# Kernel optimization log

Measured on AMD Instinct MI355X. Metric: run time of the kernel, lower is better.

Reference implementation:

```python
import jax, jax.numpy as jnp
import numpy as np

T_HORIZON = 200

def setup_inputs() -> dict:
    key = jax.random.key(0)
    ks = jax.random.split(key, 6)
    B, x_dim, kdim, u_dim = 131072, 128, 256, 64
    return {
        "x0": jax.random.normal(ks[0], (B, x_dim), jnp.float32),
        "W_phi": jax.random.normal(ks[1], (kdim, x_dim), jnp.float32) / np.float32(np.sqrt(x_dim)),
        "b_phi": jnp.zeros((kdim,), jnp.float32),
        "x_goal": jax.random.normal(ks[2], (x_dim,), jnp.float32),
        # scaled so the 200-step Riccati recursion stays numerically sane in fp32
        "phi_affine": jax.random.normal(ks[3], (kdim, kdim), jnp.float32) * np.float32(0.9 / np.sqrt(kdim)),
        "u_affine": jax.random.normal(ks[4], (kdim, u_dim), jnp.float32),
        "q_diag_log": jnp.zeros((kdim,), jnp.float32),
        "r_diag_log": jnp.zeros((u_dim,), jnp.float32),
    }

def reference(x0, W_phi, b_phi, x_goal, phi_affine, u_affine, q_diag_log, r_diag_log):
    A = phi_affine            # (k,k)
    Bm = u_affine             # (k,u)
    At, Bt = A.T, Bm.T
    Q = jnp.diag(jnp.exp(q_diag_log))   # (k,k)
    R = jnp.diag(jnp.exp(r_diag_log))   # (u,u)
    goal_g = W_phi @ x_goal + b_phi     # phi(x_goal), (k,)

    def riccati_step(carry, _):
        V, v = carry                                   # (k,k), (k,)
        M = Bt @ (V @ Bm) + R                          # (u,u)
        S = jnp.linalg.solve(M, Bt)                    # V_uu^-1 B^T, (u,k)
        K = S @ (V @ A)                                # (u,k)
        kv = S @ v                                     # (u,)
        A_BK = A - Bm @ K                              # (k,k)
        V_new = At @ (V @ A_BK) + Q
        v_new = A_BK.T @ v + Q @ goal_g
        return (V_new, v_new), (K, kv)

    (_, _), (Ks, kvs) = jax.lax.scan(riccati_step, (Q, Q @ goal_g), None, length=T_HORIZON)
    K0, k0 = Ks[-1], kvs[-1]   # last scan iter corresponds to i=0 of the reversed torch loop

    g0 = x0 @ W_phi.T + b_phi  # phi(x0), (B,k)
    u = -(g0 @ K0.T) + k0      # (B,u)
    return u
```

## Files before the change

kernel.cpp:

```cpp
#include <hip/hip_runtime.h>
#include <math.h>

#define KD 256
#define UD 64
#define XD 128

#define OFF_V     0
#define OFF_WA    65536
#define OFF_H     131072
#define OFF_G     196608
#define OFF_K0    212992
#define OFF_MI    229376
#define OFF_MP    233472
#define OFF_v     266240
#define OFF_ATV   266496
#define OFF_Z     266752
#define OFF_QG    266816
#define OFF_QD    267072
#define OFF_RD    267328
#define OFF_KV    267392
#define OFF_CV    267456
#define OFF_NKT   267520
#define DBASE     139264
#define DBUF      65536

__device__ __forceinline__ void inv4(float* D) {
#pragma unroll
  for (int p = 0; p < 4; ++p) {
    float ip = 1.0f / D[p * 4 + p];
#pragma unroll
    for (int i2 = 0; i2 < 4; ++i2)
      if (i2 != p) {
        float f = D[i2 * 4 + p] * ip;
#pragma unroll
        for (int j = 0; j < 4; ++j)
          if (j != p) D[i2 * 4 + j] -= f * D[p * 4 + j];
        D[i2 * 4 + p] = -f;
      }
#pragma unroll
    for (int j = 0; j < 4; ++j)
      if (j != p) D[p * 4 + j] *= ip;
    D[p * 4 + p] = ip;
  }
}

__device__ __forceinline__ void inv4d(double* D) {
#pragma unroll
  for (int p = 0; p < 4; ++p) {
    double ip = 1.0 / D[p * 4 + p];
#pragma unroll
    for (int i2 = 0; i2 < 4; ++i2)
      if (i2 != p) {
        double f = D[i2 * 4 + p] * ip;
#pragma unroll
        for (int j = 0; j < 4; ++j)
          if (j != p) D[i2 * 4 + j] -= f * D[p * 4 + j];
        D[i2 * 4 + p] = -f;
      }
#pragma unroll
    for (int j = 0; j < 4; ++j)
      if (j != p) D[p * 4 + j] *= ip;
    D[p * 4 + p] = ip;
  }
}

#define R16(OP) OP(0) OP(1) OP(2) OP(3) OP(4) OP(5) OP(6) OP(7) OP(8) OP(9) OP(10) OP(11) OP(12) OP(13) OP(14) OP(15)

__global__ __launch_bounds__(256) void k_init(
    const float* __restrict__ W, const float* __restrict__ bphi,
    const float* __restrict__ xg, const float* __restrict__ qlog,
    const float* __restrict__ rlog, float* __restrict__ ws)
{
  const int w = blockIdx.x, t = threadIdx.x;
  if (w < 4 && t < 64) {
    int i = w * 64 + t;
    float acc = 0.f;
    for (int p = 0; p < XD; ++p) acc = fmaf(W[i * XD + p], xg[p], acc);
    float g = acc + bphi[i];
    float qd = expf(qlog[i]);
    ws[OFF_QD + i] = qd; ws[OFF_QG + i] = qd * g; ws[OFF_v + i] = qd * g;
  }
  if (w == 4 && t < UD) ws[OFF_RD + t] = expf(rlog[t]);
}

__global__ __launch_bounds__(256) void k_cvt(
    const float* __restrict__ A, const float* __restrict__ B, float* __restrict__ ws)
{
  double* base = (double*)ws + DBASE;
  double* E1 = base + 0 * DBUF;
  double* H1 = base + 2 * DBUF;
  double* MB = base + 14 * DBUF;
  double* B64 = MB;
  double* Bs64 = MB + 16384;
  double* eA = MB + 32768;
  double* hA = MB + 33024;
  int id = blockIdx.x * 256 + threadIdx.x;
  E1[id] = (double)A[id];
  int i = id >> 8, j = id & 255;
  H1[id] = (i == j) ? (double)ws[OFF_QD + i] : 0.0;
  if (id < 16384) {
    int m = id & 63;
    B64[id] = (double)B[id];
    Bs64[id] = (double)B[id] / (double)ws[OFF_RD + m];
  }
  if (id < 256) {
    eA[id] = 0.0;
    hA[id] = -(double)ws[OFF_QG + id];
  }
}

struct GJ { const double* A; const double* B; const double* C; double* O;
            int sA0, sA1, sB0, sB1, K, addI; };
struct VJ { const double* M1; const double* x; const double* a; double* o;
            int s0, s1; double sgn; };

__global__ __launch_bounds__(256) void k_gemm64(GJ g0, GJ g1, GJ g2, int ng,
                                                VJ v0, VJ v1, VJ v2)
{
  __shared__ double As[32 * 33];
  __shared__ double Bs[32 * 33];
  __shared__ double xs[256];
  const int wg = blockIdx.x, t = threadIdx.x;
  if (wg < ng * 64) {
    GJ j = (wg < 64) ? g0 : (wg < 128) ? g1 : g2;
    const int w2 = wg & 63;
    const int tm0 = (w2 >> 3) * 32, tn0 = (w2 & 7) * 32;
    const int rq = t >> 5, c = t & 31;
    double a0 = 0, a1 = 0, a2 = 0, a3 = 0;
    for (int k0 = 0; k0 < j.K; k0 += 32) {
#pragma unroll
      for (int q = 0; q < 4; ++q) {
        int lin = q * 256 + t; int r = lin >> 5, kk = lin & 31;
        As[r * 33 + kk] = j.A[(long)(tm0 + r) * j.sA0 + (long)(k0 + kk) * j.sA1];
        Bs[r * 33 + kk] = j.B[(long)(k0 + r) * j.sB0 + (long)(tn0 + kk) * j.sB1];
      }
      __syncthreads();
#pragma unroll 8
      for (int kk = 0; kk < 32; ++kk) {
        double b = Bs[kk * 33 + c];
        a0 = fma(As[(rq * 4 + 0) * 33 + kk], b, a0);
        a1 = fma(As[(rq * 4 + 1) * 33 + kk], b, a1);
        a2 = fma(As[(rq * 4 + 2) * 33 + kk], b, a2);
        a3 = fma(As[(rq * 4 + 3) * 33 + kk], b, a3);
      }
      __syncthreads();
    }
    const int n = tn0 + c;
    double av[4] = {a0, a1, a2, a3};
#pragma unroll
    for (int i2 = 0; i2 < 4; ++i2) {
      int m = tm0 + rq * 4 + i2;
      double v = av[i2];
      if (j.C) v += j.C[m * 256 + n];
      if (j.addI && m == n) v += 1.0;
      j.O[m * 256 + n] = v;
    }
  } else {
    const int vi = wg - ng * 64;
    VJ j = (vi == 0) ? v0 : (vi == 1) ? v1 : v2;
    xs[t] = j.x[t];
    __syncthreads();
    double acc = 0;
#pragma unroll 8
    for (int k2 = 0; k2 < 256; ++k2)
      acc = fma(j.M1[(long)t * j.s0 + (long)k2 * j.s1], xs[k2], acc);
    double o = j.sgn * acc;
    if (j.a) o += j.a[t];
    j.o[t] = o;
  }
}

__global__ __launch_bounds__(256) void k_pinv(const double* __restrict__ Yc,
                                              double* __restrict__ Yn, int pk)
{
  const int w = blockIdx.x, t = threadIdx.x;
  const int bi = w >> 3, bj = w & 7;
  const int p0 = pk * 64, pb = pk * 2;
  const int r0 = bi * 32, c0 = bj * 32;

  __shared__ double sDI[64 * 65];
  __shared__ double sC [32 * 66];
  __shared__ double sR [64 * 34];
  __shared__ double sL [32 * 66];
  __shared__ double sU [64 * 34];
  __shared__ double sPR[4 * 68];
  __shared__ double sF [64 * 5];

  for (int q = 0; q < 8; ++q) { int lin = q * 256 + t; int r = lin >> 6, m = lin & 63; sC[r * 66 + m] = Yc[(r0 + r) * 256 + p0 + m]; }
  for (int q = 0; q < 8; ++q) { int lin = q * 256 + t; int m = lin >> 5, c = lin & 31; sR[m * 34 + c] = Yc[(p0 + m) * 256 + c0 + c]; }

  const int i = t & 63, cg = t >> 6;
  double rr[16];
#pragma unroll
  for (int q = 0; q < 16; ++q) rr[q] = Yc[(p0 + i) * 256 + p0 + cg * 16 + q];
  for (int k = 0; k < 16; ++k) {
    const int prw = i - 4 * k;
    const bool inblk = (unsigned)prw < 4u;
    if (inblk) {
#pragma unroll
      for (int q = 0; q < 16; ++q) sPR[prw * 68 + cg * 16 + q] = rr[q];
    }
    if (cg == (k >> 2)) {
      const int b = (k & 3) * 4;
      sF[i * 5 + 0] = rr[b + 0]; sF[i * 5 + 1] = rr[b + 1];
      sF[i * 5 + 2] = rr[b + 2]; sF[i * 5 + 3] = rr[b + 3];
    }
    __syncthreads();
    double D[16];
#pragma unroll
    for (int q = 0; q < 4; ++q) {
      D[q * 4 + 0] = sPR[q * 68 + 4 * k + 0];
      D[q * 4 + 1] = sPR[q * 68 + 4 * k + 1];
      D[q * 4 + 2] = sPR[q * 68 + 4 * k + 2];
      D[q * 4 + 3] = sPR[q * 68 + 4 * k + 3];
    }
    inv4d(D);
    double f0 = sF[i * 5 + 0], f1 = sF[i * 5 + 1], f2 = sF[i * 5 + 2], f3 = sF[i * 5 + 3];
    double g0, g1, g2, g3;
    if (inblk) {
      g0 = prw == 0 ? D[0] : prw == 1 ? D[4] : prw == 2 ? D[8]  : D[12];
      g1 = prw == 0 ? D[1] : prw == 1 ? D[5] : prw == 2 ? D[9]  : D[13];
      g2 = prw == 0 ? D[2] : prw == 1 ? D[6] : prw == 2 ? D[10] : D[14];
      g3 = prw == 0 ? D[3] : prw == 1 ? D[7] : prw == 2 ? D[11] : D[15];
    } else {
      g0 = f0 * D[0] + f1 * D[4] + f2 * D[8]  + f3 * D[12];
      g1 = f0 * D[1] + f1 * D[5] + f2 * D[9]  + f3 * D[13];
      g2 = f0 * D[2] + f1 * D[6] + f2 * D[10] + f3 * D[14];
      g3 = f0 * D[3] + f1 * D[7] + f2 * D[11] + f3 * D[15];
    }
#pragma unroll
    for (int q = 0; q < 16; ++q) {
      double pr0 = sPR[0 * 68 + cg * 16 + q];
      double pr1 = sPR[1 * 68 + cg * 16 + q];
      double pr2 = sPR[2 * 68 + cg * 16 + q];
      double pr3 = sPR[3 * 68 + cg * 16 + q];
      double n = fma(g0, pr0, fma(g1, pr1, fma(g2, pr2, g3 * pr3)));
      rr[q] = inblk ? n : rr[q] - n;
    }
    if (cg == (k >> 2)) {
      const int b = (k & 3) * 4;
      rr[b + 0] = inblk ? g0 : -g0; rr[b + 1] = inblk ? g1 : -g1;
      rr[b + 2] = inblk ? g2 : -g2; rr[b + 3] = inblk ? g3 : -g3;
    }
    __syncthreads();
  }
#pragma unroll
  for (int q = 0; q < 16; ++q) sDI[i * 65 + cg * 16 + q] = rr[q];
  __syncthreads();

  {
    const int r = t >> 3, u0 = (t & 7) * 8;
    double acc[8];
#pragma unroll
    for (int u = 0; u < 8; ++u) acc[u] = 0.0;
#pragma unroll 4
    for (int m = 0; m < 64; ++m) {
      double cv = sC[r * 66 + m];
#pragma unroll
      for (int u = 0; u < 8; ++u) acc[u] = fma(cv, sDI[m * 65 + u0 + u], acc[u]);
    }
#pragma unroll
    for (int u = 0; u < 8; ++u) sL[r * 66 + u0 + u] = acc[u];
  }
  {
    const int qrow = t >> 2, c4 = (t & 3) * 8;
    double acc[8];
#pragma unroll
    for (int u = 0; u < 8; ++u) acc[u] = 0.0;
#pragma unroll 4
    for (int m = 0; m < 64; ++m) {
      double dv = sDI[qrow * 65 + m];
#pragma unroll
      for (int u = 0; u < 8; ++u) acc[u] = fma(dv, sR[m * 34 + c4 + u], acc[u]);
    }
#pragma unroll
    for (int u = 0; u < 8; ++u) sU[qrow * 34 + c4 + u] = acc[u];
  }
  __syncthreads();

  const bool rip = (bi == pb || bi == pb + 1);
  const bool cip = (bj == pb || bj == pb + 1);
  const int r = t >> 3, cc4 = (t & 7) * 4;
#pragma unroll
  for (int u = 0; u < 4; ++u) {
    const int c = cc4 + u;
    double outv;
    if (rip && cip) {
      outv = sDI[((bi - pb) * 32 + r) * 65 + (bj - pb) * 32 + c];
    } else if (cip) {
      outv = -sL[r * 66 + (bj - pb) * 32 + c];
    } else if (rip) {
      outv = sU[((bi - pb) * 32 + r) * 34 + c];
    } else {
      double acc = Yc[(r0 + r) * 256 + c0 + c];
#pragma unroll 8
      for (int q = 0; q < 64; ++q) acc = fma(-sC[r * 66 + q], sU[q * 34 + c], acc);
      outv = acc;
    }
    Yn[(r0 + r) * 256 + c0 + c] = outv;
  }
}

__global__ __launch_bounds__(256) void k_fin2(float* __restrict__ ws)
{
  double* base = (double*)ws + DBASE;
  double* Hf = base + 8 * DBUF;
  double* hf = base + 14 * DBUF + 34048;
  int id = blockIdx.x * 256 + threadIdx.x;
  ws[OFF_V + id] = (float)Hf[id];
  if (id < 256) ws[OFF_v + id] = -(float)hf[id];
}

__global__ __launch_bounds__(256) void k_ph1(
    const float* __restrict__ A, const float* __restrict__ B,
    float* __restrict__ ws)
{
  const int u = blockIdx.x, t = threadIdx.x;
  const int sb = u & 7, hb = u >> 3;
  const int rb = sb * 32, cb0 = hb * 32, m0 = hb * 8;
  float* V   = ws + OFF_V;
  float* WAg = ws + OFF_WA;

  __shared__ float sVt[256 * 36];
  __shared__ float sA [256 * 36];
  __shared__ float sBsl[256 * 8];
  __shared__ float sBr[32 * 64];
  __shared__ float svv[256];
  __shared__ float sVB[32 * 9];
  __shared__ float sRed[8 * 36];

  for (int q = 0; q < 8; ++q) {
    int idx = q * 256 + t; int p = idx >> 3, r4 = (idx & 7) * 4;
    *(float4*)&sVt[p * 36 + r4] = *(const float4*)(V + p * KD + rb + r4);
  }
  for (int q = 0; q < 8; ++q) {
    int idx = q * 256 + t; int p = idx >> 3, r4 = (idx & 7) * 4;
    *(float4*)&sA[p * 36 + r4] = *(const float4*)(A + p * KD + cb0 + r4);
  }
  for (int q = 0; q < 2; ++q) {
    int idx = q * 256 + t; int p = idx >> 1, j4 = (idx & 1) * 4;
    *(float4*)&sBsl[p * 8 + j4] = *(const float4*)(B + p * UD + m0 + j4);
  }
  for (int q = 0; q < 2; ++q) {
    int idx = q * 256 + t; int r = idx >> 4, a4 = (idx & 15) * 4;
    *(float4*)&sBr[r * 64 + a4] = *(const float4*)(B + (rb + r) * UD + a4);
  }
  svv[t] = ws[OFF_v + t];
  __syncthreads();

  const int j = t & 31, rq = t >> 5;
  float4 acc = {0.f, 0.f, 0.f, 0.f};
  float avb0 = 0.f, avb1 = 0.f, avb2 = 0.f, avb3 = 0.f;
  const bool dovb = (j < 8);
#pragma unroll 8
  for (int p = 0; p < KD; ++p) {
    float4 v4 = *(const float4*)&sVt[p * 36 + rq * 4];
    float a = sA[p * 36 + j];
    acc.x = fmaf(v4.x, a, acc.x);
    acc.y = fmaf(v4.y, a, acc.y);
    acc.z = fmaf(v4.z, a, acc.z);
    acc.w = fmaf(v4.w, a, acc.w);
    if (dovb) {
      float b = sBsl[p * 8 + j];
      avb0 = fmaf(v4.x, b, avb0);
      avb1 = fmaf(v4.y, b, avb1);
      avb2 = fmaf(v4.z, b, avb2);
      avb3 = fmaf(v4.w, b, avb3);
    }
  }
  WAg[(rb + 4 * rq + 0) * KD + cb0 + j] = acc.x;
  WAg[(rb + 4 * rq + 1) * KD + cb0 + j] = acc.y;
  WAg[(rb + 4 * rq + 2) * KD + cb0 + j] = acc.z;
  WAg[(rb + 4 * rq + 3) * KD + cb0 + j] = acc.w;
  if (dovb) {
    sVB[(4 * rq + 0) * 9 + j] = avb0;
    sVB[(4 * rq + 1) * 9 + j] = avb1;
    sVB[(4 * rq + 2) * 9 + j] = avb2;
    sVB[(4 * rq + 3) * 9 + j] = avb3;
  }
  if (sb == 0) {
    int c = t & 31, part = t >> 5;
    float acc2 = 0.f;
#pragma unroll 8
    for (int p = part * 32; p < part * 32 + 32; ++p) acc2 = fmaf(sA[p * 36 + c], svv[p], acc2);
    sRed[part * 36 + c] = acc2;
  }
  if (sb == 1 && t < 64) {
    int jz = t & 7, part = t >> 3;
    float acc2 = 0.f;
#pragma unroll 8
    for (int p = part * 32; p < part * 32 + 32; ++p) acc2 = fmaf(sBsl[p * 8 + jz], svv[p], acc2);
    sRed[part * 36 + jz] = acc2;
  }
  __syncthreads();
  {
    int a = t & 63, j2 = (t >> 6) * 2;
    float mp0 = 0.f, mp1 = 0.f;
#pragma unroll 8
    for (int r = 0; r < 32; ++r) {
      float bv = sBr[r * 64 + a];
      mp0 = fmaf(bv, sVB[r * 9 + j2 + 0], mp0);
      mp1 = fmaf(bv, sVB[r * 9 + j2 + 1], mp1);
    }
    ws[OFF_MP + sb * 4096 + a * 64 + m0 + j2 + 0] = mp0;
    ws[OFF_MP + sb * 4096 + a * 64 + m0 + j2 + 1] = mp1;
  }
  if (sb == 0 && t < 32) {
    float a2 = 0.f;
#pragma unroll
    for (int pt = 0; pt < 8; ++pt) a2 += sRed[pt * 36 + t];
    ws[OFF_ATV + cb0 + t] = a2;
  }
  if (sb == 1 && t < 8) {
    float a2 = 0.f;
#pragma unroll
    for (int pt = 0; pt < 8; ++pt) a2 += sRed[pt * 36 + t];
    ws[OFF_Z + m0 + t] = a2;
  }
}

__global__ __launch_bounds__(256) void k_ph2(
    const float* __restrict__ A, const float* __restrict__ B,
    float* __restrict__ ws, int last)
{
  const int w = blockIdx.x, t = threadIdx.x;
  const int u = w - 1;
  float* WAg = ws + OFF_WA;
  float* MI  = ws + OFF_MI;

  __shared__ float sWA[256 * 33];
  __shared__ float sA [256 * 36];
  __shared__ float sBsl[256 * 8];
  __shared__ float scr[608];
  __shared__ float wred[256];

  if (w == 0) {
    float* sPR = scr;
    float* sF  = scr + 280;
    const int i = t & 63, cg = t >> 6;
    const float rdi = ws[OFF_RD + i];
    float rr[16];
    {
      float4 s0 = {0,0,0,0}, s1 = {0,0,0,0}, s2 = {0,0,0,0}, s3 = {0,0,0,0};
#pragma unroll
      for (int sb2 = 0; sb2 < 8; ++sb2) {
        const float* mp = ws + OFF_MP + sb2 * 4096 + i * 64 + cg * 16;
        float4 a0 = *(const float4*)(mp + 0);
        float4 a1 = *(const float4*)(mp + 4);
        float4 a2 = *(const float4*)(mp + 8);
        float4 a3 = *(const float4*)(mp + 12);
        s0.x += a0.x; s0.y += a0.y; s0.z += a0.z; s0.w += a0.w;
        s1.x += a1.x; s1.y += a1.y; s1.z += a1.z; s1.w += a1.w;
        s2.x += a2.x; s2.y += a2.y; s2.z += a2.z; s2.w += a2.w;
        s3.x += a3.x; s3.y += a3.y; s3.z += a3.z; s3.w += a3.w;
      }
      rr[0]=s0.x; rr[1]=s0.y; rr[2]=s0.z; rr[3]=s0.w;
      rr[4]=s1.x; rr[5]=s1.y; rr[6]=s1.z; rr[7]=s1.w;
      rr[8]=s2.x; rr[9]=s2.y; rr[10]=s2.z; rr[11]=s2.w;
      rr[12]=s3.x; rr[13]=s3.y; rr[14]=s3.z; rr[15]=s3.w;
#define DIAG(j) rr[j] += (cg * 16 + j == i) ? rdi : 0.f;
      R16(DIAG)
#undef DIAG
    }
    for (int k = 0; k < 16; ++k) {
      const int prw = i - 4 * k;
      const bool inblk = (unsigned)prw < 4u;
      if (inblk) {
#define ST(j) sPR[prw * 68 + cg * 16 + j] = rr[j];
        R16(ST)
#undef ST
      }
      if (cg == (k >> 2)) {
        switch (k & 3) {
          case 0: sF[i*5+0]=rr[0];  sF[i*5+1]=rr[1];  sF[i*5+2]=rr[2];  sF[i*5+3]=rr[3];  break;
          case 1: sF[i*5+0]=rr[4];  sF[i*5+1]=rr[5];  sF[i*5+2]=rr[6];  sF[i*5+3]=rr[7];  break;
          case 2: sF[i*5+0]=rr[8];  sF[i*5+1]=rr[9];  sF[i*5+2]=rr[10]; sF[i*5+3]=rr[11]; break;
          default:sF[i*5+0]=rr[12]; sF[i*5+1]=rr[13]; sF[i*5+2]=rr[14]; sF[i*5+3]=rr[15]; break;
        }
      }
      __syncthreads();
      float D[16];
#pragma unroll
      for (int q = 0; q < 4; ++q) {
        D[q*4+0] = sPR[q*68 + 4*k + 0];
        D[q*4+1] = sPR[q*68 + 4*k + 1];
        D[q*4+2] = sPR[q*68 + 4*k + 2];
        D[q*4+3] = sPR[q*68 + 4*k + 3];
      }
      inv4(D);
      float f0 = sF[i*5+0], f1 = sF[i*5+1], f2 = sF[i*5+2], f3 = sF[i*5+3];
      float g0, g1, g2, g3;
      if (inblk) {
        g0 = prw==0?D[0]:prw==1?D[4]:prw==2?D[8]:D[12];
        g1 = prw==0?D[1]:prw==1?D[5]:prw==2?D[9]:D[13];
        g2 = prw==0?D[2]:prw==1?D[6]:prw==2?D[10]:D[14];
        g3 = prw==0?D[3]:prw==1?D[7]:prw==2?D[11]:D[15];
      } else {
        g0 = f0*D[0] + f1*D[4] + f2*D[8]  + f3*D[12];
        g1 = f0*D[1] + f1*D[5] + f2*D[9]  + f3*D[13];
        g2 = f0*D[2] + f1*D[6] + f2*D[10] + f3*D[14];
        g3 = f0*D[3] + f1*D[7] + f2*D[11] + f3*D[15];
      }
#define CHUNK(c4)                                                         \
      {                                                                   \
        float4 p0 = *(const float4*)&sPR[0 * 68 + cg * 16 + (c4) * 4];    \
        float4 p1 = *(const float4*)&sPR[1 * 68 + cg * 16 + (c4) * 4];    \
        float4 p2 = *(const float4*)&sPR[2 * 68 + cg * 16 + (c4) * 4];    \
        float4 p3 = *(const float4*)&sPR[3 * 68 + cg * 16 + (c4) * 4];    \
        float n0 = fmaf(g0,p0.x, fmaf(g1,p1.x, fmaf(g2,p2.x, g3*p3.x)));  \
        float n1 = fmaf(g0,p0.y, fmaf(g1,p1.y, fmaf(g2,p2.y, g3*p3.y)));  \
        float n2 = fmaf(g0,p0.z, fmaf(g1,p1.z, fmaf(g2,p2.z, g3*p3.z)));  \
        float n3 = fmaf(g0,p0.w, fmaf(g1,p1.w, fmaf(g2,p2.w, g3*p3.w)));  \
        if (inblk) { rr[(c4)*4+0]=n0; rr[(c4)*4+1]=n1; rr[(c4)*4+2]=n2; rr[(c4)*4+3]=n3; } \
        else { rr[(c4)*4+0]-=n0; rr[(c4)*4+1]-=n1; rr[(c4)*4+2]-=n2; rr[(c4)*4+3]-=n3; }   \
      }
      CHUNK(0) CHUNK(1) CHUNK(2) CHUNK(3)
#undef CHUNK
      if (cg == (k >> 2)) {
        switch (k & 3) {
          case 0: rr[0] = inblk? g0:-g0; rr[1] = inblk? g1:-g1; rr[2] = inblk? g2:-g2; rr[3] = inblk? g3:-g3; break;
          case 1: rr[4] = inblk? g0:-g0; rr[5] = inblk? g1:-g1; rr[6] = inblk? g2:-g2; rr[7] = inblk? g3:-g3; break;
          case 2: rr[8] = inblk? g0:-g0; rr[9] = inblk? g1:-g1; rr[10]= inblk? g2:-g2; rr[11]= inblk? g3:-g3; break;
          default:rr[12]= inblk? g0:-g0; rr[13]= inblk? g1:-g1; rr[14]= inblk? g2:-g2; rr[15]= inblk? g3:-g3; break;
        }
      }
      __syncthreads();
    }
    *(float4*)(MI + i * 64 + cg * 16 + 0)  = *(float4*)&rr[0];
    *(float4*)(MI + i * 64 + cg * 16 + 4)  = *(float4*)&rr[4];
    *(float4*)(MI + i * 64 + cg * 16 + 8)  = *(float4*)&rr[8];
    *(float4*)(MI + i * 64 + cg * 16 + 12) = *(float4*)&rr[12];
    if (last) {
      float p2 = 0.f;
#define KV(j) p2 = fmaf(rr[j], ws[OFF_Z + cg * 16 + j], p2);
      R16(KV)
#undef KV
      wred[i * 4 + cg] = p2;
      __syncthreads();
      if (t < 64) ws[OFF_KV + t] = wred[t*4+0] + wred[t*4+1] + wred[t*4+2] + wred[t*4+3];
    }
  } else {
    const int sb = u & 7, hb = u >> 3;
    const int rb = sb * 32, cb0 = hb * 32, m0 = hb * 8;
    for (int q = 0; q < 8; ++q) {
      int idx = q * 256 + t;
      int p = idx >> 3, c4 = (idx & 7) * 4;
      float4 v4 = *(const float4*)(WAg + p * KD + rb + c4);
      sWA[p * 33 + c4 + 0] = v4.x;
      sWA[p * 33 + c4 + 1] = v4.y;
      sWA[p * 33 + c4 + 2] = v4.z;
      sWA[p * 33 + c4 + 3] = v4.w;
    }
    for (int q = 0; q < 8; ++q) {
      int idx = q * 256 + t; int p = idx >> 3, r4 = (idx & 7) * 4;
      *(float4*)&sA[p * 36 + r4] = *(const float4*)(A + p * KD + cb0 + r4);
    }
    for (int q = 0; q < 2; ++q) {
      int idx = q * 256 + t; int p = idx >> 1, j4 = (idx & 1) * 4;
      *(float4*)&sBsl[p * 8 + j4] = *(const float4*)(B + p * UD + m0 + j4);
    }
    __syncthreads();
    const int c = t & 31, q = t >> 5;
    float4 hacc = {0.f, 0.f, 0.f, 0.f};
    float gacc = 0.f;
#pragma unroll 8
    for (int p = 0; p < KD; ++p) {
      float wv = sWA[p * 33 + c];
      float4 a4 = *(const float4*)&sA[p * 36 + 4 * q];
      float bq = sBsl[p * 8 + q];
      hacc.x = fmaf(a4.x, wv, hacc.x);
      hacc.y = fmaf(a4.y, wv, hacc.y);
      hacc.z = fmaf(a4.z, wv, hacc.z);
      hacc.w = fmaf(a4.w, wv, hacc.w);
      gacc = fmaf(bq, wv, gacc);
    }
    float* Hm = ws + OFF_H;
    float* Gm = ws + OFF_G;
    Hm[(cb0 + 4*q + 0) * KD + rb + c] = hacc.x;
    Hm[(cb0 + 4*q + 1) * KD + rb + c] = hacc.y;
    Hm[(cb0 + 4*q + 2) * KD + rb + c] = hacc.z;
    Hm[(cb0 + 4*q + 3) * KD + rb + c] = hacc.w;
    Gm[(m0 + q) * KD + rb + c] = gacc;
  }
}

__global__ __launch_bounds__(256) void k_ph3(float* __restrict__ ws, int last)
{
  const int u = blockIdx.x, t = threadIdx.x;
  const int sb = u & 7, hb = u >> 3;
  const int cb2 = sb * 32, rb2 = hb * 32;
  float* V  = ws + OFF_V;
  float* Hm = ws + OFF_H;
  float* Gm = ws + OFF_G;

  __shared__ float sMI_[64 * 65];
  __shared__ float sGb [64 * 36];
  __shared__ float sGc [64 * 36];
  __shared__ float sKs [64 * 33];
  __shared__ float sZ[64];
  __shared__ float sQd[32];
  __shared__ float sRed[8 * 36];

  for (int q = 0; q < 16; ++q) { int idx = q * 256 + t; int row = idx >> 6, col = idx & 63; sMI_[row * 65 + col] = ws[OFF_MI + idx]; }
  for (int q = 0; q < 2; ++q) {
    int idx = q * 256 + t; int m = idx >> 3, c4 = (idx & 7) * 4;
    float4 g4 = *(const float4*)(Gm + m * KD + cb2 + c4);
    sGb[m * 36 + c4 + 0] = g4.x; sGb[m * 36 + c4 + 1] = g4.y;
    sGb[m * 36 + c4 + 2] = g4.z; sGb[m * 36 + c4 + 3] = g4.w;
  }
  for (int q = 0; q < 2; ++q) {
    int idx = q * 256 + t; int m = idx >> 3, c4 = (idx & 7) * 4;
    float4 g4 = *(const float4*)(Gm + m * KD + rb2 + c4);
    sGc[m * 36 + c4 + 0] = g4.x; sGc[m * 36 + c4 + 1] = g4.y;
    sGc[m * 36 + c4 + 2] = g4.z; sGc[m * 36 + c4 + 3] = g4.w;
  }
  if (t < 64) sZ[t] = ws[OFF_Z + t];
  if (t < 32) sQd[t] = ws[OFF_QD + rb2 + t];
  __syncthreads();
  {
    const int m = t & 63, wv = t >> 6;
    float k0=0,k1=0,k2=0,k3=0,k4=0,k5=0,k6=0,k7=0;
#pragma unroll 4
    for (int p = 0; p < UD; ++p) {
      float mi = sMI_[m * 65 + p];
      float4 ga  = *(const float4*)&sGb[p * 36 + wv * 8 + 0];
      float4 gb2 = *(const float4*)&sGb[p * 36 + wv * 8 + 4];
      k0 = fmaf(mi, ga.x, k0); k1 = fmaf(mi, ga.y, k1);
      k2 = fmaf(mi, ga.z, k2); k3 = fmaf(mi, ga.w, k3);
      k4 = fmaf(mi, gb2.x, k4); k5 = fmaf(mi, gb2.y, k5);
      k6 = fmaf(mi, gb2.z, k6); k7 = fmaf(mi, gb2.w, k7);
    }
    sKs[m * 33 + wv * 8 + 0] = k0; sKs[m * 33 + wv * 8 + 1] = k1;
    sKs[m * 33 + wv * 8 + 2] = k2; sKs[m * 33 + wv * 8 + 3] = k3;
    sKs[m * 33 + wv * 8 + 4] = k4; sKs[m * 33 + wv * 8 + 5] = k5;
    sKs[m * 33 + wv * 8 + 6] = k6; sKs[m * 33 + wv * 8 + 7] = k7;
    if (last && hb == 0) {
      float* K0 = ws + OFF_K0;
      K0[m * KD + cb2 + wv * 8 + 0] = k0; K0[m * KD + cb2 + wv * 8 + 1] = k1;
      K0[m * KD + cb2 + wv * 8 + 2] = k2; K0[m * KD + cb2 + wv * 8 + 3] = k3;
      K0[m * KD + cb2 + wv * 8 + 4] = k4; K0[m * KD + cb2 + wv * 8 + 5] = k5;
      K0[m * KD + cb2 + wv * 8 + 6] = k6; K0[m * KD + cb2 + wv * 8 + 7] = k7;
    }
  }
  __syncthreads();
  {
    const int c = t & 31, q = t >> 5;
    float a0 = 0.f, a1 = 0.f, a2 = 0.f, a3 = 0.f;
#pragma unroll 8
    for (int m = 0; m < UD; ++m) {
      float4 g4 = *(const float4*)&sGc[m * 36 + 4 * q];
      float km = sKs[m * 33 + c];
      a0 = fmaf(g4.x, km, a0); a1 = fmaf(g4.y, km, a1);
      a2 = fmaf(g4.z, km, a2); a3 = fmaf(g4.w, km, a3);
    }
    const int cc = cb2 + c;
    int r = rb2 + 4 * q;
    float h0 = Hm[(r+0) * KD + cc], h1 = Hm[(r+1) * KD + cc];
    float h2 = Hm[(r+2) * KD + cc], h3 = Hm[(r+3) * KD + cc];
    V[(r+0) * KD + cc] = h0 - a0 + ((r+0 == cc) ? sQd[4*q+0] : 0.f);
    V[(r+1) * KD + cc] = h1 - a1 + ((r+1 == cc) ? sQd[4*q+1] : 0.f);
    V[(r+2) * KD + cc] = h2 - a2 + ((r+2 == cc) ? sQd[4*q+2] : 0.f);
    V[(r+3) * KD + cc] = h3 - a3 + ((r+3 == cc) ? sQd[4*q+3] : 0.f);
  }
  if (hb == 0) {
    int c = t & 31, part = t >> 5;
    float acc2 = 0.f;
#pragma unroll
    for (int m = part * 8; m < part * 8 + 8; ++m) acc2 = fmaf(sKs[m * 33 + c], sZ[m], acc2);
    sRed[part * 36 + c] = acc2;
    __syncthreads();
    if (t < 32)  {
      float s2 = 0.f;
#pragma unroll
      for (int pt = 0; pt < 8; ++pt) s2 += sRed[pt * 36 + t];
      ws[OFF_v + cb2 + t] = ws[OFF_ATV + cb2 + t] - s2 + ws[OFF_QG + cb2 + t];
    }
  }
}

__global__ __launch_bounds__(256) void k_fin(
    const float* __restrict__ W, const float* __restrict__ bphi,
    float* __restrict__ ws)
{
  const int w = blockIdx.x, t = threadIdx.x;
  const float* K0 = ws + OFF_K0;
  if (w >= 1 && t < 128) {
    int j = t & 63, kk = 2 * (w - 1) + (t >> 6);
    float acc = 0.f;
#pragma unroll 8
    for (int i = 0; i < KD; ++i) acc = fmaf(K0[j * KD + i], W[i * XD + kk], acc);
    ws[OFF_NKT + kk * UD + j] = -acc;
  }
  if (w == 0 && t < UD) {
    float acc = 0.f;
#pragma unroll 8
    for (int i = 0; i < KD; ++i) acc = fmaf(K0[t * KD + i], bphi[i], acc);
    ws[OFF_CV + t] = ws[OFF_KV + t] - acc;
  }
}

__global__ __launch_bounds__(256) void k_batch(const float* __restrict__ x0,
                                               const float* __restrict__ ws,
                                               float* __restrict__ out)
{
  __shared__ float kt[XD][UD];
  __shared__ float cvs[UD];
  const int t = threadIdx.x;
  {
    const float4* src = (const float4*)(ws + OFF_NKT);
    float4* dst = (float4*)kt;
#pragma unroll
    for (int idx = 0; idx < (XD * UD / 4) / 256; ++idx)
      dst[t + idx * 256] = src[t + idx * 256];
  }
  if (t < UD) cvs[t] = ws[OFF_CV + t];
  __syncthreads();

  const int ty = t >> 4, tx = t & 15;
  const long r0 = (long)blockIdx.x * 64 + ty * 4;
  const float* xp = x0 + r0 * XD;

#define FMA4(acc, s, f4)                      \
  acc.x = fmaf((s), (f4).x, acc.x);           \
  acc.y = fmaf((s), (f4).y, acc.y);           \
  acc.z = fmaf((s), (f4).z, acc.z);           \
  acc.w = fmaf((s), (f4).w, acc.w);

  float4 acc0 = {0,0,0,0}, acc1 = {0,0,0,0}, acc2 = {0,0,0,0}, acc3 = {0,0,0,0};
#pragma unroll 2
  for (int k = 0; k < XD; k += 4) {
    float4 x_0 = *(const float4*)(xp + 0 * XD + k);
    float4 x_1 = *(const float4*)(xp + 1 * XD + k);
    float4 x_2 = *(const float4*)(xp + 2 * XD + k);
    float4 x_3 = *(const float4*)(xp + 3 * XD + k);
    float4 k_0 = *(const float4*)&kt[k + 0][tx * 4];
    float4 k_1 = *(const float4*)&kt[k + 1][tx * 4];
    float4 k_2 = *(const float4*)&kt[k + 2][tx * 4];
    float4 k_3 = *(const float4*)&kt[k + 3][tx * 4];
    FMA4(acc0, x_0.x, k_0) FMA4(acc0, x_0.y, k_1) FMA4(acc0, x_0.z, k_2) FMA4(acc0, x_0.w, k_3)
    FMA4(acc1, x_1.x, k_0) FMA4(acc1, x_1.y, k_1) FMA4(acc1, x_1.z, k_2) FMA4(acc1, x_1.w, k_3)
    FMA4(acc2, x_2.x, k_0) FMA4(acc2, x_2.y, k_1) FMA4(acc2, x_2.z, k_2) FMA4(acc2, x_2.w, k_3)
    FMA4(acc3, x_3.x, k_0) FMA4(acc3, x_3.y, k_1) FMA4(acc3, x_3.z, k_2) FMA4(acc3, x_3.w, k_3)
  }
  float4 cq = *(float4*)&cvs[tx * 4];
  acc0.x += cq.x; acc0.y += cq.y; acc0.z += cq.z; acc0.w += cq.w;
  acc1.x += cq.x; acc1.y += cq.y; acc1.z += cq.z; acc1.w += cq.w;
  acc2.x += cq.x; acc2.y += cq.y; acc2.z += cq.z; acc2.w += cq.w;
  acc3.x += cq.x; acc3.y += cq.y; acc3.z += cq.z; acc3.w += cq.w;
  *(float4*)(out + (r0 + 0) * UD + tx * 4) = acc0;
  *(float4*)(out + (r0 + 1) * UD + tx * 4) = acc1;
  *(float4*)(out + (r0 + 2) * UD + tx * 4) = acc2;
  *(float4*)(out + (r0 + 3) * UD + tx * 4) = acc3;
}

extern "C" void kernel_launch(void* const* d_in, const int* in_sizes, int n_in,
                              void* d_out, int out_size, void* d_ws, size_t ws_size,
                              hipStream_t stream) {
  const float* x0   = (const float*)d_in[0];
  const float* Wp   = (const float*)d_in[1];
  const float* bphi = (const float*)d_in[2];
  const float* xg   = (const float*)d_in[3];
  const float* A    = (const float*)d_in[4];
  const float* B    = (const float*)d_in[5];
  const float* ql   = (const float*)d_in[6];
  const float* rl   = (const float*)d_in[7];
  float* ws  = (float*)d_ws;
  float* out = (float*)d_out;

  double* base = (double*)d_ws + DBASE;
  double* Em[3] = { base + 0*DBUF, base + 3*DBUF, base + 6*DBUF };
  double* Gm[3] = { base + 1*DBUF, base + 4*DBUF, base + 7*DBUF };
  double* Hm[3] = { base + 2*DBUF, base + 5*DBUF, base + 8*DBUF };
  double* Wb  = base + 9*DBUF;
  double* Pb  = base + 10*DBUF;
  double* T1b = base + 11*DBUF;
  double* T2b = base + 12*DBUF;
  double* X3b = base + 13*DBUF;
  double* MB  = base + 14*DBUF;
  double* B64 = MB;
  double* Bs64= MB + 16384;
  double* ev[3] = { MB + 32768, MB + 33280, MB + 33792 };
  double* hv[3] = { MB + 33024, MB + 33536, MB + 34048 };
  double* q1  = MB + 34304;
  double* w12 = MB + 34560;
  double* u1  = MB + 34816;
  double* u2  = MB + 35072;
  double* t5  = MB + 35328;

  GJ gz{}; VJ vz{};

  hipLaunchKernelGGL(k_init, dim3(5), dim3(256), 0, stream, Wp, bphi, xg, ql, rl, ws);
  hipLaunchKernelGGL(k_cvt, dim3(256), dim3(256), 0, stream, A, B, ws);
  {
    GJ g0{ Bs64, B64, nullptr, Gm[0], 64, 1, 1, 64, 64, 0 };
    hipLaunchKernelGGL(k_gemm64, dim3(64), dim3(256), 0, stream, g0, gz, gz, 1, vz, vz, vz);
  }

  auto comp = [&](int ia, int ib, int io) {
    double *Ea = Em[ia], *Ga = Gm[ia], *Ha = Hm[ia], *ea = ev[ia], *ha = hv[ia];
    double *Eb = Em[ib], *Gb = Gm[ib], *Hb = Hm[ib], *eb = ev[ib], *hb = hv[ib];
    double *Eo = Em[io], *Go = Gm[io], *Ho = Hm[io], *eo = ev[io], *ho = hv[io];
    {
      GJ g0{ Ga, Hb, nullptr, Wb, 256, 1, 256, 1, 256, 1 };
      VJ v0{ Ga, hb, nullptr, q1, 256, 1, 1.0 };
      hipLaunchKernelGGL(k_gemm64, dim3(65), dim3(256), 0, stream, g0, gz, gz, 1, v0, vz, vz);
    }
    hipLaunchKernelGGL(k_pinv, dim3(64), dim3(256), 0, stream, Wb,  X3b, 0);
    hipLaunchKernelGGL(k_pinv, dim3(64), dim3(256), 0, stream, X3b, Wb,  1);
    hipLaunchKernelGGL(k_pinv, dim3(64), dim3(256), 0, stream, Wb,  X3b, 2);
    hipLaunchKernelGGL(k_pinv, dim3(64), dim3(256), 0, stream, X3b, Wb,  3);
    {
      GJ g0{ Wb, Ea, nullptr, Pb, 256, 1, 256, 1, 256, 0 };
      GJ g1{ Wb, Ga, nullptr, T1b, 256, 1, 256, 1, 256, 0 };
      VJ v0{ Wb, q1, nullptr, w12, 256, 1, -1.0 };
      VJ v1{ Wb, ea, nullptr, u1, 256, 1, 1.0 };
      hipLaunchKernelGGL(k_gemm64, dim3(130), dim3(256), 0, stream, g0, g1, gz, 2, v0, v1, vz);
    }
    {
      GJ g0{ Eb, Pb, nullptr, Eo, 256, 1, 256, 1, 256, 0 };
      GJ g1{ Eb, T1b, nullptr, T2b, 256, 1, 256, 1, 256, 0 };
      GJ g2{ Hb, Pb, nullptr, X3b, 256, 1, 256, 1, 256, 0 };
      VJ v0{ Eb, w12, eb, eo, 256, 1, 1.0 };
      VJ v1{ Hb, u1, nullptr, u2, 256, 1, 1.0 };
      VJ v2{ Pb, hb, ha, t5, 1, 256, 1.0 };
      hipLaunchKernelGGL(k_gemm64, dim3(195), dim3(256), 0, stream, g0, g1, g2, 3, v0, v1, v2);
    }
    {
      GJ g0{ T2b, Eb, Gb, Go, 256, 1, 1, 256, 256, 0 };
      GJ g1{ Ea, X3b, Ha, Ho, 1, 256, 256, 1, 256, 0 };
      VJ v0{ Ea, u2, t5, ho, 1, 256, 1.0 };
      hipLaunchKernelGGL(k_gemm64, dim3(129), dim3(256), 0, stream, g0, g1, gz, 2, v0, vz, vz);
    }
  };

  comp(0, 0, 1);
  comp(1, 1, 0);
  comp(0, 0, 1);
  comp(1, 1, 2);
  comp(2, 2, 0);
  comp(0, 0, 2);
  comp(2, 1, 0);
  comp(2, 2, 1);
  comp(1, 0, 2);

  hipLaunchKernelGGL(k_fin2, dim3(256), dim3(256), 0, stream, ws);
  hipLaunchKernelGGL(k_ph1, dim3(64), dim3(256), 0, stream, A, B, ws);
  hipLaunchKernelGGL(k_ph2, dim3(65), dim3(256), 0, stream, A, B, ws, 1);
  hipLaunchKernelGGL(k_ph3, dim3(64), dim3(256), 0, stream, ws, 1);
  hipLaunchKernelGGL(k_fin, dim3(65), dim3(256), 0, stream, Wp, bphi, ws);
  int rows = in_sizes[0] / XD;
  int nblk = rows / 64;
  hipLaunchKernelGGL(k_batch, dim3(nblk), dim3(256), 0, stream, x0, ws, out);
}
```

Before: 2.548 ms.

## Reassociate doubling step products to drop a serial GEMM launch per compose

The doubling-style Riccati composition is re-associated: E_a^T·H_b and G_a·E_b^T are computed up front, in parallel with the Schur-complement GEMM. That lets the final G/H updates fold into the preceding batched GEMM launch, removing one dependent launch per compose step, and the matrix-vector kernel gains a second fused matvec term. The three init launches (init, convert, B·R⁻¹·Bᵀ GEMM) merge into one seed kernel, and the batch kernel processes 128 rows per block instead of 64. The cost is extra GEMM work in the first launch and a new workspace buffer aliased into the float region, which could overlap other data.

```diff
diff --git a/kernel.cpp b/kernel.cpp
--- a/kernel.cpp
+++ b/kernel.cpp
@@ -66,53 +66,59 @@
 
 #define R16(OP) OP(0) OP(1) OP(2) OP(3) OP(4) OP(5) OP(6) OP(7) OP(8) OP(9) OP(10) OP(11) OP(12) OP(13) OP(14) OP(15)
 
-__global__ __launch_bounds__(256) void k_init(
+__global__ __launch_bounds__(256) void k_seed(
+    const float* __restrict__ A, const float* __restrict__ B,
     const float* __restrict__ W, const float* __restrict__ bphi,
     const float* __restrict__ xg, const float* __restrict__ qlog,
     const float* __restrict__ rlog, float* __restrict__ ws)
 {
-  const int w = blockIdx.x, t = threadIdx.x;
-  if (w < 4 && t < 64) {
-    int i = w * 64 + t;
-    float acc = 0.f;
-    for (int p = 0; p < XD; ++p) acc = fmaf(W[i * XD + p], xg[p], acc);
-    float g = acc + bphi[i];
-    float qd = expf(qlog[i]);
-    ws[OFF_QD + i] = qd; ws[OFF_QG + i] = qd * g; ws[OFF_v + i] = qd * g;
-  }
-  if (w == 4 && t < UD) ws[OFF_RD + t] = expf(rlog[t]);
-}
-
-__global__ __launch_bounds__(256) void k_cvt(
-    const float* __restrict__ A, const float* __restrict__ B, float* __restrict__ ws)
-{
+  __shared__ double sird[64];
   double* base = (double*)ws + DBASE;
   double* E1 = base + 0 * DBUF;
+  double* S  = base + 1 * DBUF;
   double* H1 = base + 2 * DBUF;
   double* MB = base + 14 * DBUF;
   double* B64 = MB;
   double* Bs64 = MB + 16384;
   double* eA = MB + 32768;
   double* hA = MB + 33024;
-  int id = blockIdx.x * 256 + threadIdx.x;
+  const int t = threadIdx.x;
+  if (t < 64) sird[t] = 1.0 / exp((double)rlog[t]);
+  __syncthreads();
+  const int id = blockIdx.x * 256 + t;
+  const int i = id >> 8, j = id & 255;
   E1[id] = (double)A[id];
-  int i = id >> 8, j = id & 255;
-  H1[id] = (i == j) ? (double)ws[OFF_QD + i] : 0.0;
+  H1[id] = (i == j) ? (double)expf(qlog[i]) : 0.0;
+  {
+    const float* Bi = B + i * 64;
+    const float* Bj = B + j * 64;
+    double acc = 0.0;
+#pragma unroll 8
+    for (int m = 0; m < 64; ++m)
+      acc = fma((double)Bi[m] * sird[m], (double)Bj[m], acc);
+    S[id] = acc;
+  }
   if (id < 16384) {
-    int m = id & 63;
     B64[id] = (double)B[id];
-    Bs64[id] = (double)B[id] / (double)ws[OFF_RD + m];
+    Bs64[id] = (double)B[id] * sird[id & 63];
   }
   if (id < 256) {
+    float acc = 0.f;
+    for (int p = 0; p < XD; ++p) acc = fmaf(W[id * XD + p], xg[p], acc);
+    float g = acc + bphi[id];
+    float qd = expf(qlog[id]);
+    ws[OFF_QD + id] = qd; ws[OFF_QG + id] = qd * g;
     eA[id] = 0.0;
-    hA[id] = -(double)ws[OFF_QG + id];
-  }
+    hA[id] = -(double)(qd * g);
+  }
+  if (id < 64) ws[OFF_RD + id] = expf(rlog[id]);
 }
 
 struct GJ { const double* A; const double* B; const double* C; double* O;
             int sA0, sA1, sB0, sB1, K, addI; };
 struct VJ { const double* M1; const double* x; const double* a; double* o;
-            int s0, s1; double sgn; };
+            int s0, s1; double sgn;
+            const double* M2; const double* x2; int s20, s21; double sgn2; };
 
 __global__ __launch_bounds__(256) void k_gemm64(GJ g0, GJ g1, GJ g2, int ng,
                                                 VJ v0, VJ v1, VJ v2)
@@ -120,6 +126,7 @@
   __shared__ double As[32 * 33];
   __shared__ double Bs[32 * 33];
   __shared__ double xs[256];
+  __shared__ double xs2[256];
   const int wg = blockIdx.x, t = threadIdx.x;
   if (wg < ng * 64) {
     GJ j = (wg < 64) ? g0 : (wg < 128) ? g1 : g2;
@@ -159,12 +166,20 @@
     const int vi = wg - ng * 64;
     VJ j = (vi == 0) ? v0 : (vi == 1) ? v1 : v2;
     xs[t] = j.x[t];
+    if (j.M2) xs2[t] = j.x2[t];
     __syncthreads();
     double acc = 0;
 #pragma unroll 8
     for (int k2 = 0; k2 < 256; ++k2)
       acc = fma(j.M1[(long)t * j.s0 + (long)k2 * j.s1], xs[k2], acc);
     double o = j.sgn * acc;
+    if (j.M2) {
+      double acc2 = 0;
+#pragma unroll 8
+      for (int k2 = 0; k2 < 256; ++k2)
+        acc2 = fma(j.M2[(long)t * j.s20 + (long)k2 * j.s21], xs2[k2], acc2);
+      o += j.sgn2 * acc2;
+    }
     if (j.a) o += j.a[t];
     j.o[t] = o;
   }
@@ -717,8 +732,6 @@
   __syncthreads();
 
   const int ty = t >> 4, tx = t & 15;
-  const long r0 = (long)blockIdx.x * 64 + ty * 4;
-  const float* xp = x0 + r0 * XD;
 
 #define FMA4(acc, s, f4)                      \
   acc.x = fmaf((s), (f4).x, acc.x);           \
@@ -726,31 +739,36 @@
   acc.z = fmaf((s), (f4).z, acc.z);           \
   acc.w = fmaf((s), (f4).w, acc.w);
 
-  float4 acc0 = {0,0,0,0}, acc1 = {0,0,0,0}, acc2 = {0,0,0,0}, acc3 = {0,0,0,0};
+  float4 cq = *(float4*)&cvs[tx * 4];
+#pragma unroll
+  for (int half = 0; half < 2; ++half) {
+    const long r0 = (long)blockIdx.x * 128 + half * 64 + ty * 4;
+    const float* xp = x0 + r0 * XD;
+    float4 acc0 = {0,0,0,0}, acc1 = {0,0,0,0}, acc2 = {0,0,0,0}, acc3 = {0,0,0,0};
 #pragma unroll 2
-  for (int k = 0; k < XD; k += 4) {
-    float4 x_0 = *(const float4*)(xp + 0 * XD + k);
-    float4 x_1 = *(const float4*)(xp + 1 * XD + k);
-    float4 x_2 = *(const float4*)(xp + 2 * XD + k);
-    float4 x_3 = *(const float4*)(xp + 3 * XD + k);
-    float4 k_0 = *(const float4*)&kt[k + 0][tx * 4];
-    float4 k_1 = *(const float4*)&kt[k + 1][tx * 4];
-    float4 k_2 = *(const float4*)&kt[k + 2][tx * 4];
-    float4 k_3 = *(const float4*)&kt[k + 3][tx * 4];
-    FMA4(acc0, x_0.x, k_0) FMA4(acc0, x_0.y, k_1) FMA4(acc0, x_0.z, k_2) FMA4(acc0, x_0.w, k_3)
-    FMA4(acc1, x_1.x, k_0) FMA4(acc1, x_1.y, k_1) FMA4(acc1, x_1.z, k_2) FMA4(acc1, x_1.w, k_3)
-    FMA4(acc2, x_2.x, k_0) FMA4(acc2, x_2.y, k_1) FMA4(acc2, x_2.z, k_2) FMA4(acc2, x_2.w, k_3)
-    FMA4(acc3, x_3.x, k_0) FMA4(acc3, x_3.y, k_1) FMA4(acc3, x_3.z, k_2) FMA4(acc3, x_3.w, k_3)
-  }
-  float4 cq = *(float4*)&cvs[tx * 4];
-  acc0.x += cq.x; acc0.y += cq.y; acc0.z += cq.z; acc0.w += cq.w;
-  acc1.x += cq.x; acc1.y += cq.y; acc1.z += cq.z; acc1.w += cq.w;
-  acc2.x += cq.x; acc2.y += cq.y; acc2.z += cq.z; acc2.w += cq.w;
-  acc3.x += cq.x; acc3.y += cq.y; acc3.z += cq.z; acc3.w += cq.w;
-  *(float4*)(out + (r0 + 0) * UD + tx * 4) = acc0;
-  *(float4*)(out + (r0 + 1) * UD + tx * 4) = acc1;
-  *(float4*)(out + (r0 + 2) * UD + tx * 4) = acc2;
-  *(float4*)(out + (r0 + 3) * UD + tx * 4) = acc3;
+    for (int k = 0; k < XD; k += 4) {
+      float4 x_0 = *(const float4*)(xp + 0 * XD + k);
+      float4 x_1 = *(const float4*)(xp + 1 * XD + k);
+      float4 x_2 = *(const float4*)(xp + 2 * XD + k);
+      float4 x_3 = *(const float4*)(xp + 3 * XD + k);
+      float4 k_0 = *(const float4*)&kt[k + 0][tx * 4];
+      float4 k_1 = *(const float4*)&kt[k + 1][tx * 4];
+      float4 k_2 = *(const float4*)&kt[k + 2][tx * 4];
+      float4 k_3 = *(const float4*)&kt[k + 3][tx * 4];
+      FMA4(acc0, x_0.x, k_0) FMA4(acc0, x_0.y, k_1) FMA4(acc0, x_0.z, k_2) FMA4(acc0, x_0.w, k_3)
+      FMA4(acc1, x_1.x, k_0) FMA4(acc1, x_1.y, k_1) FMA4(acc1, x_1.z, k_2) FMA4(acc1, x_1.w, k_3)
+      FMA4(acc2, x_2.x, k_0) FMA4(acc2, x_2.y, k_1) FMA4(acc2, x_2.z, k_2) FMA4(acc2, x_2.w, k_3)
+      FMA4(acc3, x_3.x, k_0) FMA4(acc3, x_3.y, k_1) FMA4(acc3, x_3.z, k_2) FMA4(acc3, x_3.w, k_3)
+    }
+    acc0.x += cq.x; acc0.y += cq.y; acc0.z += cq.z; acc0.w += cq.w;
+    acc1.x += cq.x; acc1.y += cq.y; acc1.z += cq.z; acc1.w += cq.w;
+    acc2.x += cq.x; acc2.y += cq.y; acc2.z += cq.z; acc2.w += cq.w;
+    acc3.x += cq.x; acc3.y += cq.y; acc3.z += cq.z; acc3.w += cq.w;
+    *(float4*)(out + (r0 + 0) * UD + tx * 4) = acc0;
+    *(float4*)(out + (r0 + 1) * UD + tx * 4) = acc1;
+    *(float4*)(out + (r0 + 2) * UD + tx * 4) = acc2;
+    *(float4*)(out + (r0 + 3) * UD + tx * 4) = acc3;
+  }
 }
 
 extern "C" void kernel_launch(void* const* d_in, const int* in_sizes, int n_in,
@@ -774,27 +792,20 @@
   double* Wb  = base + 9*DBUF;
   double* Pb  = base + 10*DBUF;
   double* T1b = base + 11*DBUF;
-  double* T2b = base + 12*DBUF;
+  double* Jb  = base + 12*DBUF;
   double* X3b = base + 13*DBUF;
+  double* Nb  = (double*)d_ws + 32768;
   double* MB  = base + 14*DBUF;
-  double* B64 = MB;
-  double* Bs64= MB + 16384;
   double* ev[3] = { MB + 32768, MB + 33280, MB + 33792 };
   double* hv[3] = { MB + 33024, MB + 33536, MB + 34048 };
   double* q1  = MB + 34304;
   double* w12 = MB + 34560;
   double* u1  = MB + 34816;
-  double* u2  = MB + 35072;
-  double* t5  = MB + 35328;
 
   GJ gz{}; VJ vz{};
 
-  hipLaunchKernelGGL(k_init, dim3(5), dim3(256), 0, stream, Wp, bphi, xg, ql, rl, ws);
-  hipLaunchKernelGGL(k_cvt, dim3(256), dim3(256), 0, stream, A, B, ws);
-  {
-    GJ g0{ Bs64, B64, nullptr, Gm[0], 64, 1, 1, 64, 64, 0 };
-    hipLaunchKernelGGL(k_gemm64, dim3(64), dim3(256), 0, stream, g0, gz, gz, 1, vz, vz, vz);
-  }
+  hipLaunchKernelGGL(k_seed, dim3(256), dim3(256), 0, stream,
+                     A, B, Wp, bphi, xg, ql, rl, ws);
 
   auto comp = [&](int ia, int ib, int io) {
     double *Ea = Em[ia], *Ga = Gm[ia], *Ha = Hm[ia], *ea = ev[ia], *ha = hv[ia];
@@ -802,8 +813,10 @@
     double *Eo = Em[io], *Go = Gm[io], *Ho = Hm[io], *eo = ev[io], *ho = hv[io];
     {
       GJ g0{ Ga, Hb, nullptr, Wb, 256, 1, 256, 1, 256, 1 };
+      GJ g1{ Ea, Hb, nullptr, Jb, 1, 256, 256, 1, 256, 0 };
+      GJ g2{ Ga, Eb, nullptr, Nb, 256, 1, 1, 256, 256, 0 };
       VJ v0{ Ga, hb, nullptr, q1, 256, 1, 1.0 };
-      hipLaunchKernelGGL(k_gemm64, dim3(65), dim3(256), 0, stream, g0, gz, gz, 1, v0, vz, vz);
+      hipLaunchKernelGGL(k_gemm64, dim3(193), dim3(256), 0, stream, g0, g1, g2, 3, v0, vz, vz);
     }
     hipLaunchKernelGGL(k_pinv, dim3(64), dim3(256), 0, stream, Wb,  X3b, 0);
     hipLaunchKernelGGL(k_pinv, dim3(64), dim3(256), 0, stream, X3b, Wb,  1);
@@ -811,25 +824,18 @@
     hipLaunchKernelGGL(k_pinv, dim3(64), dim3(256), 0, stream, X3b, Wb,  3);
     {
       GJ g0{ Wb, Ea, nullptr, Pb, 256, 1, 256, 1, 256, 0 };
-      GJ g1{ Wb, Ga, nullptr, T1b, 256, 1, 256, 1, 256, 0 };
+      GJ g1{ Wb, Nb, nullptr, T1b, 256, 1, 256, 1, 256, 0 };
       VJ v0{ Wb, q1, nullptr, w12, 256, 1, -1.0 };
       VJ v1{ Wb, ea, nullptr, u1, 256, 1, 1.0 };
       hipLaunchKernelGGL(k_gemm64, dim3(130), dim3(256), 0, stream, g0, g1, gz, 2, v0, v1, vz);
     }
     {
       GJ g0{ Eb, Pb, nullptr, Eo, 256, 1, 256, 1, 256, 0 };
-      GJ g1{ Eb, T1b, nullptr, T2b, 256, 1, 256, 1, 256, 0 };
-      GJ g2{ Hb, Pb, nullptr, X3b, 256, 1, 256, 1, 256, 0 };
+      GJ g1{ Eb, T1b, Gb, Go, 256, 1, 256, 1, 256, 0 };
+      GJ g2{ Jb, Pb, Ha, Ho, 256, 1, 256, 1, 256, 0 };
       VJ v0{ Eb, w12, eb, eo, 256, 1, 1.0 };
-      VJ v1{ Hb, u1, nullptr, u2, 256, 1, 1.0 };
-      VJ v2{ Pb, hb, ha, t5, 1, 256, 1.0 };
-      hipLaunchKernelGGL(k_gemm64, dim3(195), dim3(256), 0, stream, g0, g1, g2, 3, v0, v1, v2);
-    }
-    {
-      GJ g0{ T2b, Eb, Gb, Go, 256, 1, 1, 256, 256, 0 };
-      GJ g1{ Ea, X3b, Ha, Ho, 1, 256, 256, 1, 256, 0 };
-      VJ v0{ Ea, u2, t5, ho, 1, 256, 1.0 };
-      hipLaunchKernelGGL(k_gemm64, dim3(129), dim3(256), 0, stream, g0, g1, gz, 2, v0, vz, vz);
+      VJ v1{ Jb, u1, ha, ho, 256, 1, 1.0, Pb, hb, 1, 256, 1.0 };
+      hipLaunchKernelGGL(k_gemm64, dim3(194), dim3(256), 0, stream, g0, g1, g2, 3, v0, v1, vz);
     }
   };
 
@@ -849,6 +855,6 @@
   hipLaunchKernelGGL(k_ph3, dim3(64), dim3(256), 0, stream, ws, 1);
   hipLaunchKernelGGL(k_fin, dim3(65), dim3(256), 0, stream, Wp, bphi, ws);
   int rows = in_sizes[0] / XD;
-  int nblk = rows / 64;
+  int nblk = rows / 128;
   hipLaunchKernelGGL(k_batch, dim3(nblk), dim3(256), 0, stream, x0, ws, out);
 }
```

Result: faster. 2.479 ms (-2.7%).
